# Kernel tuning notes

Hardware: AMD Instinct MI355X
Metric: run time of the kernel (lower is better)

## Reference

```python
import jax, jax.numpy as jnp
import numpy as np

B, T, M, D = 8, 256, 64, 512
H = 8
DK = D // H


def setup_inputs() -> dict:
    key = jax.random.key(0)
    ks = jax.random.split(key, 9)
    s = 1.0 / np.sqrt(D)
    return {
        "x": jax.random.normal(ks[0], (B, T, M, D), dtype=jnp.float32),
        "Wq": jax.random.normal(ks[1], (D, D), dtype=jnp.float32) * s,
        "bq": jax.random.normal(ks[2], (D,), dtype=jnp.float32) * s,
        "Wk": jax.random.normal(ks[3], (D, D), dtype=jnp.float32) * s,
        "bk": jax.random.normal(ks[4], (D,), dtype=jnp.float32) * s,
        "Wv": jax.random.normal(ks[5], (D, D), dtype=jnp.float32) * s,
        "bv": jax.random.normal(ks[6], (D,), dtype=jnp.float32) * s,
        "Wo": jax.random.normal(ks[7], (D, D), dtype=jnp.float32) * s,
        "bo": jax.random.normal(ks[8], (D,), dtype=jnp.float32) * s,
    }


def reference(x, Wq, bq, Wk, bk, Wv, bv, Wo, bo):
    # x: (B, T, M, D); attention over the M (units) axis per (B, T, head).
    scale = jnp.asarray(np.sqrt(DK), dtype=x.dtype)
    q = (x @ Wq.T + bq).reshape(B, T, M, H, DK)
    k = (x @ Wk.T + bk).reshape(B, T, M, H, DK)
    v = (x @ Wv.T + bv).reshape(B, T, M, H, DK)
    # scores: (B, T, H, M, M)
    scores = jnp.einsum("btqhd,btkhd->bthqk", q, k) / scale
    attn = jax.nn.softmax(scores, axis=-1)  # dropout is identity in eval
    out = jnp.einsum("bthqk,btkhd->btqhd", attn, v).reshape(B, T, M, D)
    return out @ Wo.T + bo
```

## Files before the change

kernel.cpp:

```cpp
#include <hip/hip_runtime.h>


typedef unsigned short u16;
typedef short s4v __attribute__((ext_vector_type(4)));
typedef short s8v __attribute__((ext_vector_type(8)));
typedef unsigned short us4 __attribute__((ext_vector_type(4)));
typedef __bf16 bf8v __attribute__((ext_vector_type(8)));
typedef float f4v __attribute__((ext_vector_type(4)));
typedef float fl4 __attribute__((ext_vector_type(4)));

#define LX 516
#define LQ 68
#define LB 36

static __device__ __forceinline__ u16 f2bf(float f) {
  union { float f; unsigned u; } v;
  v.f = f;
  unsigned r = v.u + 0x7fffu + ((v.u >> 16) & 1u);
  return (u16)(r >> 16);
}

union Frag8 { s4v h[2]; s8v v; };

static __device__ __forceinline__ s8v load_frag(const u16* p) {
  Frag8 f;
  f.h[0] = *(const s4v*)(p);
  f.h[1] = *(const s4v*)(p + 4);
  return f.v;
}

static __device__ __forceinline__ f4v mfma16(s8v a, s8v b, f4v c) {
  return __builtin_amdgcn_mfma_f32_16x16x32_bf16(
      __builtin_bit_cast(bf8v, a), __builtin_bit_cast(bf8v, b), c, 0, 0, 0);
}

__global__ __launch_bounds__(256) void pack_weights_kernel(
    const float* __restrict__ Wq, const float* __restrict__ Wk,
    const float* __restrict__ Wv, const float* __restrict__ Wo,
    u16* __restrict__ Wqkv, u16* __restrict__ Wob) {
  const int i4 = (blockIdx.x * 256 + threadIdx.x) * 4;
  fl4 a = *(const fl4*)(Wq + i4);
  fl4 b = *(const fl4*)(Wk + i4);
  fl4 c = *(const fl4*)(Wv + i4);
  fl4 d = *(const fl4*)(Wo + i4);
  us4 pa, pb, pc, pd;
#pragma unroll
  for (int t = 0; t < 4; ++t) {
    pa[t] = f2bf(a[t]); pb[t] = f2bf(b[t]);
    pc[t] = f2bf(c[t]); pd[t] = f2bf(d[t]);
  }
  *(us4*)(Wqkv + i4) = pa;
  *(us4*)(Wqkv + 262144 + i4) = pb;
  *(us4*)(Wqkv + 524288 + i4) = pc;
  *(us4*)(Wob + i4) = pd;
}

__global__ __launch_bounds__(512) void qkv_attn_kernel(
    const float* __restrict__ x, const u16* __restrict__ Wqkv,
    const float* __restrict__ bq, const float* __restrict__ bk,
    const float* __restrict__ bv, u16* __restrict__ attn) {
  __shared__ u16 x_s[64 * LX];
  __shared__ u16 qs[2][64 * LQ];
  __shared__ u16 ks_[2][64 * LQ];
  __shared__ u16 vs[2][64 * LQ];
  __shared__ u16 Ps[2][64 * LQ];

  const int bt = blockIdx.x;
  const int tid = threadIdx.x;
  const int lane = tid & 63;
  const int wave = tid >> 6;
  const int grp = wave >> 2;
  const int w = wave & 3;
  const int l15 = lane & 15;
  const int l4 = lane >> 4;

  {
    const float* xp = x + (size_t)bt * (64 * 512);
    const int c4 = (tid & 127) * 4;
    const int r0 = tid >> 7;
#pragma unroll
    for (int i = 0; i < 16; ++i) {
      const int r = r0 + i * 4;
      fl4 v = *(const fl4*)(xp + r * 512 + c4);
      us4 p;
      p[0] = f2bf(v[0]); p[1] = f2bf(v[1]);
      p[2] = f2bf(v[2]); p[3] = f2bf(v[3]);
      *(us4*)&x_s[r * LX + c4] = p;
    }
  }
  __syncthreads();

  const f4v fzero = {0.f, 0.f, 0.f, 0.f};

  for (int hi = 0; hi < 4; ++hi) {
    const int h = grp * 4 + hi;
    const int ncol = h * 64 + 16 * w + l15;
    const float bqv = bq[ncol];
    const float bkv = bk[ncol];
    const float bvv = bv[ncol];
    const u16* WqP = Wqkv + (size_t)ncol * 512 + l4 * 8;
    const u16* WkP = Wqkv + (size_t)(512 + ncol) * 512 + l4 * 8;
    const u16* WvP = Wqkv + (size_t)(1024 + ncol) * 512 + l4 * 8;

    f4v aq[4], ak[4], av[4];
#pragma unroll
    for (int i = 0; i < 4; ++i) { aq[i] = fzero; ak[i] = fzero; av[i] = fzero; }

#pragma unroll
    for (int kk = 0; kk < 16; ++kk) {
      const int ko = kk * 32 + l4 * 8;
      const s8v bq8 = *(const s8v*)(WqP + kk * 32);
      const s8v bk8 = *(const s8v*)(WkP + kk * 32);
      const s8v bv8 = *(const s8v*)(WvP + kk * 32);
      const s8v a0 = load_frag(&x_s[(0 + l15) * LX + ko]);
      const s8v a1 = load_frag(&x_s[(16 + l15) * LX + ko]);
      const s8v a2 = load_frag(&x_s[(32 + l15) * LX + ko]);
      const s8v a3 = load_frag(&x_s[(48 + l15) * LX + ko]);
      aq[0] = mfma16(a0, bq8, aq[0]); aq[1] = mfma16(a1, bq8, aq[1]);
      aq[2] = mfma16(a2, bq8, aq[2]); aq[3] = mfma16(a3, bq8, aq[3]);
      ak[0] = mfma16(a0, bk8, ak[0]); ak[1] = mfma16(a1, bk8, ak[1]);
      ak[2] = mfma16(a2, bk8, ak[2]); ak[3] = mfma16(a3, bk8, ak[3]);
      av[0] = mfma16(a0, bv8, av[0]); av[1] = mfma16(a1, bv8, av[1]);
      av[2] = mfma16(a2, bv8, av[2]); av[3] = mfma16(a3, bv8, av[3]);
    }

    const int nl = 16 * w + l15;
#pragma unroll
    for (int i = 0; i < 4; ++i) {
#pragma unroll
      for (int r = 0; r < 4; ++r) {
        const int m = 16 * i + 4 * l4 + r;
        qs[grp][m * LQ + nl] = f2bf((aq[i][r] + bqv) * 0.125f);
        ks_[grp][m * LQ + nl] = f2bf(ak[i][r] + bkv);
        vs[grp][nl * LQ + m] = f2bf(av[i][r] + bvv);
      }
    }
    __syncthreads();

    f4v s[4];
#pragma unroll
    for (int j = 0; j < 4; ++j) s[j] = fzero;
#pragma unroll
    for (int kc = 0; kc < 2; ++kc) {
      const s8v af = load_frag(&qs[grp][(16 * w + l15) * LQ + kc * 32 + l4 * 8]);
#pragma unroll
      for (int j = 0; j < 4; ++j) {
        const s8v bf = load_frag(&ks_[grp][(16 * j + l15) * LQ + kc * 32 + l4 * 8]);
        s[j] = mfma16(af, bf, s[j]);
      }
    }
#pragma unroll
    for (int r = 0; r < 4; ++r) {
      float mx = fmaxf(fmaxf(s[0][r], s[1][r]), fmaxf(s[2][r], s[3][r]));
      mx = fmaxf(mx, __shfl_xor(mx, 1));
      mx = fmaxf(mx, __shfl_xor(mx, 2));
      mx = fmaxf(mx, __shfl_xor(mx, 4));
      mx = fmaxf(mx, __shfl_xor(mx, 8));
      float e0 = __expf(s[0][r] - mx);
      float e1 = __expf(s[1][r] - mx);
      float e2 = __expf(s[2][r] - mx);
      float e3 = __expf(s[3][r] - mx);
      float sm = e0 + e1 + e2 + e3;
      sm += __shfl_xor(sm, 1);
      sm += __shfl_xor(sm, 2);
      sm += __shfl_xor(sm, 4);
      sm += __shfl_xor(sm, 8);
      const float inv = __builtin_amdgcn_rcpf(sm);
      s[0][r] = e0 * inv; s[1][r] = e1 * inv;
      s[2][r] = e2 * inv; s[3][r] = e3 * inv;
    }
#pragma unroll
    for (int j = 0; j < 4; ++j)
#pragma unroll
      for (int r = 0; r < 4; ++r)
        Ps[grp][(16 * w + 4 * l4 + r) * LQ + 16 * j + l15] = f2bf(s[j][r]);
    __syncthreads();

    f4v o[4];
#pragma unroll
    for (int j = 0; j < 4; ++j) o[j] = fzero;
#pragma unroll
    for (int kc = 0; kc < 2; ++kc) {
      const s8v af = load_frag(&Ps[grp][(16 * w + l15) * LQ + kc * 32 + l4 * 8]);
#pragma unroll
      for (int j = 0; j < 4; ++j) {
        const s8v bf = load_frag(&vs[grp][(16 * j + l15) * LQ + kc * 32 + l4 * 8]);
        o[j] = mfma16(af, bf, o[j]);
      }
    }
    u16* ap = attn + (size_t)(bt * 64) * 512 + h * 64;
#pragma unroll
    for (int j = 0; j < 4; ++j)
#pragma unroll
      for (int r = 0; r < 4; ++r)
        ap[(size_t)(16 * w + 4 * l4 + r) * 512 + 16 * j + l15] = f2bf(o[j][r]);
    __syncthreads();
  }
}

__global__ __launch_bounds__(256) void out_proj_kernel(
    const u16* __restrict__ attn, const u16* __restrict__ Wob,
    const float* __restrict__ bo, float* __restrict__ out) {
  __shared__ u16 As[128 * LB];
  __shared__ u16 Bs[128 * LB];
  const int m0 = blockIdx.x * 128;
  const int n0 = blockIdx.y * 128;
  const int tid = threadIdx.x;
  const int lane = tid & 63;
  const int wave = tid >> 6;
  const int wy = wave >> 1;
  const int wx = wave & 1;
  const int l15 = lane & 15;
  const int l4 = lane >> 4;

  const f4v fzero = {0.f, 0.f, 0.f, 0.f};
  f4v acc[4][4];
#pragma unroll
  for (int i = 0; i < 4; ++i)
#pragma unroll
    for (int j = 0; j < 4; ++j) acc[i][j] = fzero;

  const int row0 = tid >> 2, cc0 = (tid & 3) * 8;
  const int c1 = tid + 256;
  const int row1 = c1 >> 2, cc1 = (c1 & 3) * 8;

  for (int k0 = 0; k0 < 512; k0 += 32) {
    __syncthreads();
    {
      Frag8 ga0, gb0, ga1, gb1;
      ga0.v = *(const s8v*)(attn + (size_t)(m0 + row0) * 512 + k0 + cc0);
      gb0.v = *(const s8v*)(Wob + (size_t)(n0 + row0) * 512 + k0 + cc0);
      ga1.v = *(const s8v*)(attn + (size_t)(m0 + row1) * 512 + k0 + cc1);
      gb1.v = *(const s8v*)(Wob + (size_t)(n0 + row1) * 512 + k0 + cc1);
      *(s4v*)&As[row0 * LB + cc0] = ga0.h[0];
      *(s4v*)&As[row0 * LB + cc0 + 4] = ga0.h[1];
      *(s4v*)&Bs[row0 * LB + cc0] = gb0.h[0];
      *(s4v*)&Bs[row0 * LB + cc0 + 4] = gb0.h[1];
      *(s4v*)&As[row1 * LB + cc1] = ga1.h[0];
      *(s4v*)&As[row1 * LB + cc1 + 4] = ga1.h[1];
      *(s4v*)&Bs[row1 * LB + cc1] = gb1.h[0];
      *(s4v*)&Bs[row1 * LB + cc1 + 4] = gb1.h[1];
    }
    __syncthreads();
    s8v a[4], b[4];
#pragma unroll
    for (int i = 0; i < 4; ++i)
      a[i] = load_frag(&As[(wy * 64 + 16 * i + l15) * LB + l4 * 8]);
#pragma unroll
    for (int j = 0; j < 4; ++j)
      b[j] = load_frag(&Bs[(wx * 64 + 16 * j + l15) * LB + l4 * 8]);
#pragma unroll
    for (int i = 0; i < 4; ++i)
#pragma unroll
      for (int j = 0; j < 4; ++j)
        acc[i][j] = mfma16(a[i], b[j], acc[i][j]);
  }
#pragma unroll
  for (int j = 0; j < 4; ++j) {
    const int col = n0 + wx * 64 + 16 * j + l15;
    const float bb = bo[col];
#pragma unroll
    for (int i = 0; i < 4; ++i) {
#pragma unroll
      for (int r = 0; r < 4; ++r) {
        const int row = m0 + wy * 64 + 16 * i + 4 * l4 + r;
        out[(size_t)row * 512 + col] = acc[i][j][r] + bb;
      }
    }
  }
}

extern "C" void kernel_launch(void* const* d_in, const int* in_sizes, int n_in,
                              void* d_out, int out_size, void* d_ws, size_t ws_size,
                              hipStream_t stream) {
  const float* x  = (const float*)d_in[0];
  const float* Wq = (const float*)d_in[1];
  const float* bq = (const float*)d_in[2];
  const float* Wk = (const float*)d_in[3];
  const float* bk = (const float*)d_in[4];
  const float* Wv = (const float*)d_in[5];
  const float* bv = (const float*)d_in[6];
  const float* Wo = (const float*)d_in[7];
  const float* bo = (const float*)d_in[8];
  float* out = (float*)d_out;

  u16* Wqkv = (u16*)d_ws;
  u16* Wob  = Wqkv + 3 * 512 * 512;
  u16* attn = Wob + 512 * 512;

  pack_weights_kernel<<<256, 256, 0, stream>>>(Wq, Wk, Wv, Wo, Wqkv, Wob);
  qkv_attn_kernel<<<2048, 512, 0, stream>>>(x, Wqkv, bq, bk, bv, attn);
  out_proj_kernel<<<dim3(1024, 4), 256, 0, stream>>>(attn, Wob, bo, out);
}
```

Before: 1.009 ms.

## Stage x through global bf16 scratch, drop big LDS tile, async LDS loads in out-proj

The QKV/attention kernel no longer holds the 64x512 x tile in LDS. It converts x to bf16 into the attn output buffer in global memory and reads the MFMA A-fragments directly from global/L2. This cuts LDS use so more blocks can be resident (launch bounds 512,4), and P reuses the q buffer, dropping one barrier. Attention outputs stay in registers across the four heads and are written back over the same scratch area at the end. The out-projection kernel switches to global_load_lds async copies with unpadded LDS tiles. The risks are higher global/L2 traffic for the A operand, bank conflicts from removing the padding, and a possible race if another block or wave reads the scratch before it is overwritten.

```diff
diff --git a/kernel.cpp b/kernel.cpp
--- a/kernel.cpp
+++ b/kernel.cpp
@@ -2,16 +2,14 @@
 
 
 typedef unsigned short u16;
-typedef short s4v __attribute__((ext_vector_type(4)));
 typedef short s8v __attribute__((ext_vector_type(8)));
 typedef unsigned short us4 __attribute__((ext_vector_type(4)));
+typedef unsigned short us8 __attribute__((ext_vector_type(8)));
 typedef __bf16 bf8v __attribute__((ext_vector_type(8)));
 typedef float f4v __attribute__((ext_vector_type(4)));
 typedef float fl4 __attribute__((ext_vector_type(4)));
 
-#define LX 516
-#define LQ 68
-#define LB 36
+#define LQ 72
 
 static __device__ __forceinline__ u16 f2bf(float f) {
   union { float f; unsigned u; } v;
@@ -20,19 +18,19 @@
   return (u16)(r >> 16);
 }
 
-union Frag8 { s4v h[2]; s8v v; };
-
-static __device__ __forceinline__ s8v load_frag(const u16* p) {
-  Frag8 f;
-  f.h[0] = *(const s4v*)(p);
-  f.h[1] = *(const s4v*)(p + 4);
-  return f.v;
+static __device__ __forceinline__ s8v ld16(const u16* p) {
+  return *(const s8v*)p;
 }
 
 static __device__ __forceinline__ f4v mfma16(s8v a, s8v b, f4v c) {
   return __builtin_amdgcn_mfma_f32_16x16x32_bf16(
       __builtin_bit_cast(bf8v, a), __builtin_bit_cast(bf8v, b), c, 0, 0, 0);
 }
+
+#define ASYNC16(g, l)                                                  \
+  __builtin_amdgcn_global_load_lds(                                    \
+      (const __attribute__((address_space(1))) void*)(g),              \
+      (__attribute__((address_space(3))) void*)(l), 16, 0, 0)
 
 __global__ __launch_bounds__(256) void pack_weights_kernel(
     const float* __restrict__ Wq, const float* __restrict__ Wk,
@@ -55,15 +53,13 @@
   *(us4*)(Wob + i4) = pd;
 }
 
-__global__ __launch_bounds__(512) void qkv_attn_kernel(
+__global__ __launch_bounds__(512, 4) void qkv_attn_kernel(
     const float* __restrict__ x, const u16* __restrict__ Wqkv,
     const float* __restrict__ bq, const float* __restrict__ bk,
     const float* __restrict__ bv, u16* __restrict__ attn) {
-  __shared__ u16 x_s[64 * LX];
   __shared__ u16 qs[2][64 * LQ];
   __shared__ u16 ks_[2][64 * LQ];
   __shared__ u16 vs[2][64 * LQ];
-  __shared__ u16 Ps[2][64 * LQ];
 
   const int bt = blockIdx.x;
   const int tid = threadIdx.x;
@@ -74,24 +70,25 @@
   const int l15 = lane & 15;
   const int l4 = lane >> 4;
 
-  {
-    const float* xp = x + (size_t)bt * (64 * 512);
-    const int c4 = (tid & 127) * 4;
-    const int r0 = tid >> 7;
-#pragma unroll
-    for (int i = 0; i < 16; ++i) {
-      const int r = r0 + i * 4;
-      fl4 v = *(const fl4*)(xp + r * 512 + c4);
-      us4 p;
-      p[0] = f2bf(v[0]); p[1] = f2bf(v[1]);
-      p[2] = f2bf(v[2]); p[3] = f2bf(v[3]);
-      *(us4*)&x_s[r * LX + c4] = p;
-    }
+  const float* xp = x + (size_t)bt * 32768;
+  u16* xb = attn + (size_t)bt * 32768;
+
+#pragma unroll
+  for (int i = 0; i < 8; ++i) {
+    const int idx = i * 4096 + tid * 8;
+    fl4 a = *(const fl4*)(xp + idx);
+    fl4 b = *(const fl4*)(xp + idx + 4);
+    us8 p;
+    p[0] = f2bf(a[0]); p[1] = f2bf(a[1]); p[2] = f2bf(a[2]); p[3] = f2bf(a[3]);
+    p[4] = f2bf(b[0]); p[5] = f2bf(b[1]); p[6] = f2bf(b[2]); p[7] = f2bf(b[3]);
+    *(us8*)(xb + idx) = p;
   }
   __syncthreads();
 
   const f4v fzero = {0.f, 0.f, 0.f, 0.f};
-
+  unsigned opk[4][8];
+
+#pragma unroll
   for (int hi = 0; hi < 4; ++hi) {
     const int h = grp * 4 + hi;
     const int ncol = h * 64 + 16 * w + l15;
@@ -106,16 +103,16 @@
 #pragma unroll
     for (int i = 0; i < 4; ++i) { aq[i] = fzero; ak[i] = fzero; av[i] = fzero; }
 
-#pragma unroll
+#pragma unroll 4
     for (int kk = 0; kk < 16; ++kk) {
       const int ko = kk * 32 + l4 * 8;
-      const s8v bq8 = *(const s8v*)(WqP + kk * 32);
-      const s8v bk8 = *(const s8v*)(WkP + kk * 32);
-      const s8v bv8 = *(const s8v*)(WvP + kk * 32);
-      const s8v a0 = load_frag(&x_s[(0 + l15) * LX + ko]);
-      const s8v a1 = load_frag(&x_s[(16 + l15) * LX + ko]);
-      const s8v a2 = load_frag(&x_s[(32 + l15) * LX + ko]);
-      const s8v a3 = load_frag(&x_s[(48 + l15) * LX + ko]);
+      const s8v bq8 = ld16(WqP + kk * 32);
+      const s8v bk8 = ld16(WkP + kk * 32);
+      const s8v bv8 = ld16(WvP + kk * 32);
+      const s8v a0 = ld16(xb + (0 + l15) * 512 + ko);
+      const s8v a1 = ld16(xb + (16 + l15) * 512 + ko);
+      const s8v a2 = ld16(xb + (32 + l15) * 512 + ko);
+      const s8v a3 = ld16(xb + (48 + l15) * 512 + ko);
       aq[0] = mfma16(a0, bq8, aq[0]); aq[1] = mfma16(a1, bq8, aq[1]);
       aq[2] = mfma16(a2, bq8, aq[2]); aq[3] = mfma16(a3, bq8, aq[3]);
       ak[0] = mfma16(a0, bk8, ak[0]); ak[1] = mfma16(a1, bk8, ak[1]);
@@ -142,10 +139,10 @@
     for (int j = 0; j < 4; ++j) s[j] = fzero;
 #pragma unroll
     for (int kc = 0; kc < 2; ++kc) {
-      const s8v af = load_frag(&qs[grp][(16 * w + l15) * LQ + kc * 32 + l4 * 8]);
+      const s8v af = ld16(&qs[grp][(16 * w + l15) * LQ + kc * 32 + l4 * 8]);
 #pragma unroll
       for (int j = 0; j < 4; ++j) {
-        const s8v bf = load_frag(&ks_[grp][(16 * j + l15) * LQ + kc * 32 + l4 * 8]);
+        const s8v bf = ld16(&ks_[grp][(16 * j + l15) * LQ + kc * 32 + l4 * 8]);
         s[j] = mfma16(af, bf, s[j]);
       }
     }
@@ -169,50 +166,69 @@
       s[0][r] = e0 * inv; s[1][r] = e1 * inv;
       s[2][r] = e2 * inv; s[3][r] = e3 * inv;
     }
+    u16* Ps = qs[grp];
 #pragma unroll
     for (int j = 0; j < 4; ++j)
 #pragma unroll
       for (int r = 0; r < 4; ++r)
-        Ps[grp][(16 * w + 4 * l4 + r) * LQ + 16 * j + l15] = f2bf(s[j][r]);
-    __syncthreads();
+        Ps[(16 * w + 4 * l4 + r) * LQ + 16 * j + l15] = f2bf(s[j][r]);
 
     f4v o[4];
 #pragma unroll
     for (int j = 0; j < 4; ++j) o[j] = fzero;
 #pragma unroll
     for (int kc = 0; kc < 2; ++kc) {
-      const s8v af = load_frag(&Ps[grp][(16 * w + l15) * LQ + kc * 32 + l4 * 8]);
+      const s8v af = ld16(&Ps[(16 * w + l15) * LQ + kc * 32 + l4 * 8]);
 #pragma unroll
       for (int j = 0; j < 4; ++j) {
-        const s8v bf = load_frag(&vs[grp][(16 * j + l15) * LQ + kc * 32 + l4 * 8]);
+        const s8v bf = ld16(&vs[grp][(16 * j + l15) * LQ + kc * 32 + l4 * 8]);
         o[j] = mfma16(af, bf, o[j]);
       }
     }
-    u16* ap = attn + (size_t)(bt * 64) * 512 + h * 64;
-#pragma unroll
-    for (int j = 0; j < 4; ++j)
-#pragma unroll
-      for (int r = 0; r < 4; ++r)
-        ap[(size_t)(16 * w + 4 * l4 + r) * 512 + 16 * j + l15] = f2bf(o[j][r]);
-    __syncthreads();
+#pragma unroll
+    for (int j = 0; j < 4; ++j) {
+      opk[hi][j * 2 + 0] = (unsigned)f2bf(o[j][0]) | ((unsigned)f2bf(o[j][1]) << 16);
+      opk[hi][j * 2 + 1] = (unsigned)f2bf(o[j][2]) | ((unsigned)f2bf(o[j][3]) << 16);
+    }
+    __syncthreads();
+  }
+
+#pragma unroll
+  for (int hi = 0; hi < 4; ++hi) {
+    const int h = grp * 4 + hi;
+#pragma unroll
+    for (int j = 0; j < 4; ++j) {
+#pragma unroll
+      for (int t = 0; t < 2; ++t) {
+        const unsigned v = opk[hi][j * 2 + t];
+        const int m = 16 * w + 4 * l4 + 2 * t;
+        xb[(size_t)m * 512 + h * 64 + 16 * j + l15] = (u16)(v & 0xffffu);
+        xb[(size_t)(m + 1) * 512 + h * 64 + 16 * j + l15] = (u16)(v >> 16);
+      }
+    }
   }
 }
 
 __global__ __launch_bounds__(256) void out_proj_kernel(
     const u16* __restrict__ attn, const u16* __restrict__ Wob,
     const float* __restrict__ bo, float* __restrict__ out) {
-  __shared__ u16 As[128 * LB];
-  __shared__ u16 Bs[128 * LB];
+  __shared__ u16 As[128 * 32];
+  __shared__ u16 Bs[128 * 32];
+  const int tid = threadIdx.x;
+  const int lane = tid & 63;
+  const int wv = tid >> 6;
   const int m0 = blockIdx.x * 128;
   const int n0 = blockIdx.y * 128;
-  const int tid = threadIdx.x;
-  const int lane = tid & 63;
-  const int wave = tid >> 6;
-  const int wy = wave >> 1;
-  const int wx = wave & 1;
+  const int wy = wv >> 1;
+  const int wx = wv & 1;
   const int l15 = lane & 15;
   const int l4 = lane >> 4;
 
+  const u16* gA = attn + (size_t)(m0 + 16 * wv + (lane >> 2)) * 512 + (lane & 3) * 8;
+  const u16* gB = Wob + (size_t)(n0 + 16 * wv + (lane >> 2)) * 512 + (lane & 3) * 8;
+  u16* lA = As + wv * 512;
+  u16* lB = Bs + wv * 512;
+
   const f4v fzero = {0.f, 0.f, 0.f, 0.f};
   f4v acc[4][4];
 #pragma unroll
@@ -220,35 +236,20 @@
 #pragma unroll
     for (int j = 0; j < 4; ++j) acc[i][j] = fzero;
 
-  const int row0 = tid >> 2, cc0 = (tid & 3) * 8;
-  const int c1 = tid + 256;
-  const int row1 = c1 >> 2, cc1 = (c1 & 3) * 8;
-
   for (int k0 = 0; k0 < 512; k0 += 32) {
     __syncthreads();
-    {
-      Frag8 ga0, gb0, ga1, gb1;
-      ga0.v = *(const s8v*)(attn + (size_t)(m0 + row0) * 512 + k0 + cc0);
-      gb0.v = *(const s8v*)(Wob + (size_t)(n0 + row0) * 512 + k0 + cc0);
-      ga1.v = *(const s8v*)(attn + (size_t)(m0 + row1) * 512 + k0 + cc1);
-      gb1.v = *(const s8v*)(Wob + (size_t)(n0 + row1) * 512 + k0 + cc1);
-      *(s4v*)&As[row0 * LB + cc0] = ga0.h[0];
-      *(s4v*)&As[row0 * LB + cc0 + 4] = ga0.h[1];
-      *(s4v*)&Bs[row0 * LB + cc0] = gb0.h[0];
-      *(s4v*)&Bs[row0 * LB + cc0 + 4] = gb0.h[1];
-      *(s4v*)&As[row1 * LB + cc1] = ga1.h[0];
-      *(s4v*)&As[row1 * LB + cc1 + 4] = ga1.h[1];
-      *(s4v*)&Bs[row1 * LB + cc1] = gb1.h[0];
-      *(s4v*)&Bs[row1 * LB + cc1 + 4] = gb1.h[1];
-    }
+    ASYNC16(gA + k0, lA);
+    ASYNC16(gA + 64 * 512 + k0, lA + 2048);
+    ASYNC16(gB + k0, lB);
+    ASYNC16(gB + 64 * 512 + k0, lB + 2048);
     __syncthreads();
     s8v a[4], b[4];
 #pragma unroll
     for (int i = 0; i < 4; ++i)
-      a[i] = load_frag(&As[(wy * 64 + 16 * i + l15) * LB + l4 * 8]);
+      a[i] = ld16(&As[(wy * 64 + 16 * i + l15) * 32 + l4 * 8]);
 #pragma unroll
     for (int j = 0; j < 4; ++j)
-      b[j] = load_frag(&Bs[(wx * 64 + 16 * j + l15) * LB + l4 * 8]);
+      b[j] = ld16(&Bs[(wx * 64 + 16 * j + l15) * 32 + l4 * 8]);
 #pragma unroll
     for (int i = 0; i < 4; ++i)
 #pragma unroll
```

New measurement: 1.388 ms. 37.6% more time.
